# Performance work log

Hardware: AMD Instinct MI355X
Metric: run time of the kernel (lower is better)

Reference implementation:

```python
import jax, jax.numpy as jnp
import numpy as np

D_REP = 128        # node_representation_size
N_TYPES = 10000    # unique_internal_nodes (Internal_Node_Impact rows)
G = 2000           # number of external-graph nodes (internal graphs)
K = 64             # internal nodes per internal graph
DEG_IN = 8         # internal neighbour degree
DEG_EXT = 16       # external neighbour degree
B = 1024           # batch of node-id pairs


def setup_inputs() -> dict:
    key = jax.random.key(0)
    ks = jax.random.split(key, 16)
    def xavier(k, shape):
        fan_in, fan_out = shape[-1], shape[-2] if len(shape) > 1 else shape[-1]
        std = float(np.sqrt(2.0 / (fan_in + fan_out)))
        return jax.random.normal(k, shape, dtype=jnp.float32) * std
    return {
        # graph structure (integer constants)
        "batch": jax.random.randint(ks[0], (B, 2), 0, G),
        "node_type": jax.random.randint(ks[1], (G, K), 0, N_TYPES),
        "nbr_type": jax.random.randint(ks[2], (G, K, DEG_IN), 0, N_TYPES),
        "ext_nbr": jax.random.randint(ks[3], (G, DEG_EXT), 0, G),
        # InternalGraphConvolutionLayer params
        "impact": xavier(ks[4], (N_TYPES, D_REP)),   # Internal_Node_Impact
        "W": xavier(ks[5], (D_REP, D_REP)),
        "M": xavier(ks[6], (D_REP, D_REP)),
        # ExternalGraphConvolutionLayer params
        "U": xavier(ks[7], (D_REP, D_REP)),
        "V": xavier(ks[8], (D_REP, D_REP)),
        # LinkPredictionLayer params
        "W1": xavier(ks[9], (D_REP, 2 * D_REP)),
        "b1": jnp.zeros((D_REP,), dtype=jnp.float32),
        "W2": xavier(ks[10], (2, D_REP)),
        "b2": jnp.zeros((2,), dtype=jnp.float32),
    }


def reference(batch, node_type, nbr_type, ext_nbr, impact, W, M, U, V, W1, b1, W2, b2):
    # ---- InternalGraphConvolutionLayer, batched over all G graphs ----
    # per node: W @ impact[type] + sum_nbr M @ impact[nbr_type]
    self_msg = impact[node_type] @ W.T                    # [G,K,d]
    nbr_msg = impact[nbr_type].sum(axis=2) @ M.T          # gather [G,K,Din,d] -> [G,K,d]
    per_graph = jax.nn.relu(self_msg + nbr_msg).sum(axis=1)  # sum over internal nodes -> [G,d]
    E = jax.nn.softmax(per_graph, axis=-1)                # [G,d] internal embedding

    # ---- ExternalGraphConvolutionLayer, batched over all G nodes ----
    ext = E @ U.T + E[ext_nbr].sum(axis=1) @ V.T          # U@e_i + sum_j V@e_j  [G,d]
    X = jax.nn.softmax(jax.nn.relu(ext), axis=-1)         # [G,d] external embedding

    # ---- LinkPredictionLayer on each batch pair ----
    e1 = X[batch[:, 0]]                                   # [B,d]
    e2 = X[batch[:, 1]]                                   # [B,d]
    feat = jnp.concatenate([e1 * e2, e1 + e2], axis=-1)   # [B,2d]
    h = jax.nn.relu(feat @ W1.T + b1)                     # [B,d]
    return jax.nn.softmax(h @ W2.T + b2, axis=-1)         # [B,2]
```

## Files before the change

kernel.cpp:

```cpp
#include <hip/hip_runtime.h>

typedef __bf16 bf16x8 __attribute__((ext_vector_type(8)));
typedef float f32x4 __attribute__((ext_vector_type(4)));

#define G_N 2000
#define K_N 64
#define DEG_INN 8
#define DEG_EXTN 16
#define B_N 1024
#define D 128
#define NT_N 10000

__device__ __forceinline__ float bflo(unsigned int u) { return __uint_as_float(u << 16); }
__device__ __forceinline__ float bfhi(unsigned int u) { return __uint_as_float(u & 0xffff0000u); }
__device__ __forceinline__ unsigned short f2bf(float f) {
  unsigned int u = __float_as_uint(f);
  u += 0x7fffu + ((u >> 16) & 1u);
  return (unsigned short)(u >> 16);
}
__device__ __forceinline__ unsigned int pack2bf(float lo, float hi) {
  return ((unsigned int)f2bf(hi) << 16) | (unsigned int)f2bf(lo);
}

constexpr int LD1 = 136;

__global__ __launch_bounds__(256)
void k0_prep(const float* __restrict__ impact,
             const float* __restrict__ Wm, const float* __restrict__ Mm,
             const float* __restrict__ U, const float* __restrict__ V,
             const float* __restrict__ W1,
             unsigned int* __restrict__ P, unsigned int* __restrict__ Q,
             unsigned int* __restrict__ Ut, unsigned int* __restrict__ Vt,
             unsigned int* __restrict__ W1t)
{
  __shared__ __align__(16) unsigned short Bs[128 * LD1];
  __shared__ __align__(16) unsigned short As[64 * LD1];

  const int tid = threadIdx.x;

  if (blockIdx.y == 2) {
    if (blockIdx.x >= 64) return;
    const int t = blockIdx.x * 256 + tid;
    if (t < 8192) {
      int k = t >> 6, jc = t & 63;
      Ut[t] = pack2bf(U[(size_t)(2 * jc) * D + k], U[(size_t)(2 * jc + 1) * D + k]);
      Vt[t] = pack2bf(V[(size_t)(2 * jc) * D + k], V[(size_t)(2 * jc + 1) * D + k]);
    }
    {
      int k = t >> 6, jc = t & 63;
      W1t[t] = pack2bf(W1[(size_t)(2 * jc) * 256 + k], W1[(size_t)(2 * jc + 1) * 256 + k]);
    }
    return;
  }

  const int rowbase = blockIdx.x * 64;
  const float* Bsrc = blockIdx.y ? Mm : Wm;
  unsigned int* dst = blockIdx.y ? Q : P;
  const int wave = tid >> 6, lane = tid & 63;

  for (int i = tid; i < 128 * 32; i += 256) {
    int row = i >> 5, c4 = i & 31;
    float4 v = ((const float4*)Bsrc)[row * 32 + c4];
    *(unsigned int*)(Bs + row * LD1 + c4 * 4)     = pack2bf(v.x, v.y);
    *(unsigned int*)(Bs + row * LD1 + c4 * 4 + 2) = pack2bf(v.z, v.w);
  }
  for (int i = tid; i < 64 * 32; i += 256) {
    int r = i >> 5, c4 = i & 31;
    int gr = rowbase + r; if (gr > NT_N - 1) gr = NT_N - 1;
    float4 v = ((const float4*)impact)[(size_t)gr * 32 + c4];
    *(unsigned int*)(As + r * LD1 + c4 * 4)     = pack2bf(v.x, v.y);
    *(unsigned int*)(As + r * LD1 + c4 * 4 + 2) = pack2bf(v.z, v.w);
  }
  __syncthreads();

  f32x4 acc[8];
  #pragma unroll
  for (int n = 0; n < 8; ++n) acc[n] = (f32x4){0.f, 0.f, 0.f, 0.f};
  const int qk   = (lane >> 4) * 8;
  const int arow = wave * 16 + (lane & 15);
  #pragma unroll
  for (int kk = 0; kk < 4; ++kk) {
    bf16x8 af = *(const bf16x8*)(As + arow * LD1 + kk * 32 + qk);
    #pragma unroll
    for (int n = 0; n < 8; ++n) {
      bf16x8 bfr = *(const bf16x8*)(Bs + (n * 16 + (lane & 15)) * LD1 + kk * 32 + qk);
      acc[n] = __builtin_amdgcn_mfma_f32_16x16x32_bf16(af, bfr, acc[n], 0, 0, 0);
    }
  }
  __syncthreads();

  const int quad = lane >> 4, c = lane & 15;
  #pragma unroll
  for (int n = 0; n < 8; ++n)
    #pragma unroll
    for (int reg = 0; reg < 4; ++reg)
      As[(wave * 16 + quad * 4 + reg) * LD1 + n * 16 + c] = f2bf(acc[n][reg]);
  __syncthreads();

  for (int i = tid; i < 64 * 32; i += 256) {
    int r = i >> 5, cc = i & 31;
    int gr = rowbase + r;
    if (gr < NT_N) {
      dst[(size_t)gr * 64 + cc * 2]     = *(unsigned int*)(As + r * LD1 + cc * 4);
      dst[(size_t)gr * 64 + cc * 2 + 1] = *(unsigned int*)(As + r * LD1 + cc * 4 + 2);
    }
  }
}

__global__ __launch_bounds__(256)
void k1_gather(const int* __restrict__ node_type, const int* __restrict__ nbr_type,
               const uint4* __restrict__ P, const uint4* __restrict__ Q,
               float* __restrict__ E)
{
  __shared__ int nts[64];
  __shared__ int nbs[512];
  __shared__ float rg[16][132];
  __shared__ float pg[128];

  const int g    = blockIdx.x;
  const int tid  = threadIdx.x;
  const int wave = tid >> 6, lane = tid & 63;
  const int slot = lane >> 4, cl = lane & 15;

  if (tid < 64) nts[tid] = node_type[g * K_N + tid];
  nbs[tid]       = nbr_type[(size_t)g * 512 + tid];
  nbs[256 + tid] = nbr_type[(size_t)g * 512 + 256 + tid];
  __syncthreads();

  float acc[8];
  #pragma unroll
  for (int i = 0; i < 8; ++i) acc[i] = 0.f;

  for (int it = 0; it < 4; ++it) {
    const int r = wave * 16 + it * 4 + slot;
    uint4 sv = P[(size_t)nts[r] * 16 + cl];
    float rv[8];
    rv[0] = bflo(sv.x); rv[1] = bfhi(sv.x); rv[2] = bflo(sv.y); rv[3] = bfhi(sv.y);
    rv[4] = bflo(sv.z); rv[5] = bfhi(sv.z); rv[6] = bflo(sv.w); rv[7] = bfhi(sv.w);
    const int* nb = nbs + r * DEG_INN;
    #pragma unroll
    for (int d = 0; d < DEG_INN; ++d) {
      uint4 qv = Q[(size_t)nb[d] * 16 + cl];
      rv[0] += bflo(qv.x); rv[1] += bfhi(qv.x); rv[2] += bflo(qv.y); rv[3] += bfhi(qv.y);
      rv[4] += bflo(qv.z); rv[5] += bfhi(qv.z); rv[6] += bflo(qv.w); rv[7] += bfhi(qv.w);
    }
    #pragma unroll
    for (int i = 0; i < 8; ++i) acc[i] += fmaxf(rv[i], 0.f);
  }

  const int grp = wave * 4 + slot;
  #pragma unroll
  for (int i = 0; i < 8; ++i) rg[grp][cl * 8 + i] = acc[i];
  __syncthreads();

  if (tid < 128) {
    float s = 0.f;
    #pragma unroll
    for (int q = 0; q < 16; ++q) s += rg[q][tid];
    pg[tid] = s;
  }
  __syncthreads();

  if (wave == 0) {
    float v0 = pg[lane], v1 = pg[64 + lane];
    float mx = fmaxf(v0, v1);
    #pragma unroll
    for (int o = 32; o; o >>= 1) mx = fmaxf(mx, __shfl_xor(mx, o, 64));
    float e0 = __expf(v0 - mx), e1 = __expf(v1 - mx);
    float s = e0 + e1;
    #pragma unroll
    for (int o = 32; o; o >>= 1) s += __shfl_xor(s, o, 64);
    float inv = 1.f / s;
    E[(size_t)g * D + lane]      = e0 * inv;
    E[(size_t)g * D + 64 + lane] = e1 * inv;
  }
}

__global__ __launch_bounds__(256)
void k3_ext(const int* __restrict__ ext_nbr, const float* __restrict__ E,
            const unsigned int* __restrict__ Ut, const unsigned int* __restrict__ Vt,
            float* __restrict__ X)
{
  __shared__ float Ev[128], Es[128];
  __shared__ float p0[4][64], p1[4][64];
  __shared__ float scr[8];
  __shared__ int en[16];

  const int g   = blockIdx.x;
  const int tid = threadIdx.x;
  const int jc  = tid & 63, grp = tid >> 6;
  const int lane = tid & 63, wv = tid >> 6;

  if (tid < 16) en[tid] = ext_nbr[g * DEG_EXTN + tid];
  __syncthreads();

  if (tid < 128) {
    Ev[tid] = E[(size_t)g * D + tid];
  } else {
    const int j = tid - 128;
    float a = 0.f;
    #pragma unroll
    for (int d = 0; d < DEG_EXTN; ++d) a += E[(size_t)en[d] * D + j];
    Es[j] = a;
  }
  __syncthreads();

  const unsigned int* T = (grp & 2) ? Vt : Ut;
  const float* act      = (grp & 2) ? Es : Ev;
  const int k0 = (grp & 1) * 64;
  float s0 = 0.f, s1 = 0.f;
  #pragma unroll 16
  for (int k = 0; k < 64; ++k) {
    unsigned int uu = T[(k0 + k) * 64 + jc];
    float a = act[k0 + k];
    s0 += bflo(uu) * a; s1 += bfhi(uu) * a;
  }
  p0[grp][jc] = s0; p1[grp][jc] = s1;
  __syncthreads();

  float r = 0.f, e = 0.f;
  if (tid < 128) {
    const int jc2 = tid >> 1;
    float v = (tid & 1) ? (p1[0][jc2] + p1[1][jc2] + p1[2][jc2] + p1[3][jc2])
                        : (p0[0][jc2] + p0[1][jc2] + p0[2][jc2] + p0[3][jc2]);
    r = fmaxf(v, 0.f);
    float mx = r;
    #pragma unroll
    for (int o = 32; o; o >>= 1) mx = fmaxf(mx, __shfl_xor(mx, o, 64));
    if (lane == 0) scr[wv] = mx;
  }
  __syncthreads();
  if (tid < 128) {
    float mx = fmaxf(scr[0], scr[1]);
    e = __expf(r - mx);
    float sm = e;
    #pragma unroll
    for (int o = 32; o; o >>= 1) sm += __shfl_xor(sm, o, 64);
    if (lane == 0) scr[4 + wv] = sm;
  }
  __syncthreads();
  if (tid < 128) X[(size_t)g * D + tid] = e / (scr[4] + scr[5]);
}

__global__ __launch_bounds__(256)
void k4_mlp(const int* __restrict__ batch, const float* __restrict__ Xv,
            const unsigned int* __restrict__ W1t, const float* __restrict__ b1,
            const float* __restrict__ W2, const float* __restrict__ b2,
            float* __restrict__ out)
{
  __shared__ float feat[256];
  __shared__ float q0[4][64], q1[4][64];
  __shared__ float hv[128];
  __shared__ float scr[2];

  const int tid = threadIdx.x;
  const int jc = tid & 63, grp = tid >> 6;
  const int lane = tid & 63, wv = tid >> 6;

  for (int it = 0; it < 2; ++it) {
    const int b = blockIdx.x * 2 + it;
    const int i1 = batch[2 * b], i2 = batch[2 * b + 1];
    if (tid < 128) {
      float e1 = Xv[(size_t)i1 * D + tid], e2 = Xv[(size_t)i2 * D + tid];
      feat[tid]       = e1 * e2;
      feat[128 + tid] = e1 + e2;
    }
    __syncthreads();

    float s0 = 0.f, s1 = 0.f;
    #pragma unroll 16
    for (int k = 0; k < 64; ++k) {
      unsigned int uu = W1t[(grp * 64 + k) * 64 + jc];
      float a = feat[grp * 64 + k];
      s0 += bflo(uu) * a; s1 += bfhi(uu) * a;
    }
    q0[grp][jc] = s0; q1[grp][jc] = s1;
    __syncthreads();

    if (tid < 128) {
      const int jc2 = tid >> 1;
      float h = (tid & 1) ? (q1[0][jc2] + q1[1][jc2] + q1[2][jc2] + q1[3][jc2])
                          : (q0[0][jc2] + q0[1][jc2] + q0[2][jc2] + q0[3][jc2]);
      hv[tid] = fmaxf(h + b1[tid], 0.f);
    }
    __syncthreads();

    if (wv < 2) {
      float p = W2[wv * 128 + lane] * hv[lane]
              + W2[wv * 128 + 64 + lane] * hv[64 + lane];
      #pragma unroll
      for (int o = 32; o; o >>= 1) p += __shfl_xor(p, o, 64);
      if (lane == 0) scr[wv] = p + b2[wv];
    }
    __syncthreads();
    if (tid == 0) {
      float r0 = scr[0], r1 = scr[1];
      float m = fmaxf(r0, r1);
      float e0 = __expf(r0 - m), e1 = __expf(r1 - m);
      float inv = 1.f / (e0 + e1);
      out[2 * b]     = e0 * inv;
      out[2 * b + 1] = e1 * inv;
    }
    __syncthreads();
  }
}

extern "C" void kernel_launch(void* const* d_in, const int* in_sizes, int n_in,
                              void* d_out, int out_size, void* d_ws, size_t ws_size,
                              hipStream_t stream) {
  const int* batch     = (const int*)d_in[0];
  const int* node_type = (const int*)d_in[1];
  const int* nbr_type  = (const int*)d_in[2];
  const int* ext_nbr   = (const int*)d_in[3];
  const float* impact  = (const float*)d_in[4];
  const float* W       = (const float*)d_in[5];
  const float* M       = (const float*)d_in[6];
  const float* U       = (const float*)d_in[7];
  const float* V       = (const float*)d_in[8];
  const float* W1      = (const float*)d_in[9];
  const float* b1      = (const float*)d_in[10];
  const float* W2      = (const float*)d_in[11];
  const float* b2      = (const float*)d_in[12];
  float* out           = (float*)d_out;

  float* E = (float*)d_ws;
  float* X = E + (size_t)G_N * D;
  unsigned int* P   = (unsigned int*)(X + (size_t)G_N * D);
  unsigned int* Q   = P + (size_t)NT_N * 64;
  unsigned int* Ut  = Q + (size_t)NT_N * 64;
  unsigned int* Vt  = Ut + 8192;
  unsigned int* W1t = Vt + 8192;

  k0_prep<<<dim3((NT_N + 63) / 64, 3), 256, 0, stream>>>(impact, W, M, U, V, W1,
                                                         P, Q, Ut, Vt, W1t);
  k1_gather<<<G_N, 256, 0, stream>>>(node_type, nbr_type,
                                     (const uint4*)P, (const uint4*)Q, E);
  k3_ext<<<G_N, 256, 0, stream>>>(ext_nbr, E, Ut, Vt, X);
  k4_mlp<<<B_N / 2, 256, 0, stream>>>(batch, X, W1t, b1, W2, b2, out);
}
```

Before: 134.9 us.

## Fuse W/M projections per block and cache weight columns in registers

The prep kernel now loads each impact tile once and computes both the W and M projections from it, instead of launching separate blocks per matrix. The external-conv and MLP kernels keep their slice of the transposed weight matrix in 64 registers and loop over four graphs or pairs per block. The neighbour sum is also split across all 256 threads. This is meant to cut repeated global weight reads and redundant impact loads, at the cost of higher register pressure and fewer blocks in flight.

```diff
diff --git a/kernel.cpp b/kernel.cpp
--- a/kernel.cpp
+++ b/kernel.cpp
@@ -38,9 +38,8 @@
 
   const int tid = threadIdx.x;
 
-  if (blockIdx.y == 2) {
-    if (blockIdx.x >= 64) return;
-    const int t = blockIdx.x * 256 + tid;
+  if (blockIdx.x >= 157) {
+    const int t = (blockIdx.x - 157) * 256 + tid;
     if (t < 8192) {
       int k = t >> 6, jc = t & 63;
       Ut[t] = pack2bf(U[(size_t)(2 * jc) * D + k], U[(size_t)(2 * jc + 1) * D + k]);
@@ -54,16 +53,11 @@
   }
 
   const int rowbase = blockIdx.x * 64;
-  const float* Bsrc = blockIdx.y ? Mm : Wm;
-  unsigned int* dst = blockIdx.y ? Q : P;
   const int wave = tid >> 6, lane = tid & 63;
-
-  for (int i = tid; i < 128 * 32; i += 256) {
-    int row = i >> 5, c4 = i & 31;
-    float4 v = ((const float4*)Bsrc)[row * 32 + c4];
-    *(unsigned int*)(Bs + row * LD1 + c4 * 4)     = pack2bf(v.x, v.y);
-    *(unsigned int*)(Bs + row * LD1 + c4 * 4 + 2) = pack2bf(v.z, v.w);
-  }
+  const int qk   = (lane >> 4) * 8;
+  const int arow = wave * 16 + (lane & 15);
+  const int quad = lane >> 4, c = lane & 15;
+
   for (int i = tid; i < 64 * 32; i += 256) {
     int r = i >> 5, c4 = i & 31;
     int gr = rowbase + r; if (gr > NT_N - 1) gr = NT_N - 1;
@@ -71,38 +65,78 @@
     *(unsigned int*)(As + r * LD1 + c4 * 4)     = pack2bf(v.x, v.y);
     *(unsigned int*)(As + r * LD1 + c4 * 4 + 2) = pack2bf(v.z, v.w);
   }
-  __syncthreads();
-
-  f32x4 acc[8];
-  #pragma unroll
-  for (int n = 0; n < 8; ++n) acc[n] = (f32x4){0.f, 0.f, 0.f, 0.f};
-  const int qk   = (lane >> 4) * 8;
-  const int arow = wave * 16 + (lane & 15);
+  for (int i = tid; i < 128 * 32; i += 256) {
+    int row = i >> 5, c4 = i & 31;
+    float4 v = ((const float4*)Wm)[row * 32 + c4];
+    *(unsigned int*)(Bs + row * LD1 + c4 * 4)     = pack2bf(v.x, v.y);
+    *(unsigned int*)(Bs + row * LD1 + c4 * 4 + 2) = pack2bf(v.z, v.w);
+  }
+  __syncthreads();
+
+  f32x4 accW[8], accM[8];
+  #pragma unroll
+  for (int n = 0; n < 8; ++n) accW[n] = (f32x4){0.f, 0.f, 0.f, 0.f};
+  #pragma unroll
+  for (int n = 0; n < 8; ++n) accM[n] = (f32x4){0.f, 0.f, 0.f, 0.f};
+
   #pragma unroll
   for (int kk = 0; kk < 4; ++kk) {
     bf16x8 af = *(const bf16x8*)(As + arow * LD1 + kk * 32 + qk);
     #pragma unroll
     for (int n = 0; n < 8; ++n) {
       bf16x8 bfr = *(const bf16x8*)(Bs + (n * 16 + (lane & 15)) * LD1 + kk * 32 + qk);
-      acc[n] = __builtin_amdgcn_mfma_f32_16x16x32_bf16(af, bfr, acc[n], 0, 0, 0);
-    }
-  }
-  __syncthreads();
-
-  const int quad = lane >> 4, c = lane & 15;
+      accW[n] = __builtin_amdgcn_mfma_f32_16x16x32_bf16(af, bfr, accW[n], 0, 0, 0);
+    }
+  }
+  __syncthreads();
+
+  for (int i = tid; i < 128 * 32; i += 256) {
+    int row = i >> 5, c4 = i & 31;
+    float4 v = ((const float4*)Mm)[row * 32 + c4];
+    *(unsigned int*)(Bs + row * LD1 + c4 * 4)     = pack2bf(v.x, v.y);
+    *(unsigned int*)(Bs + row * LD1 + c4 * 4 + 2) = pack2bf(v.z, v.w);
+  }
+  __syncthreads();
+
+  #pragma unroll
+  for (int kk = 0; kk < 4; ++kk) {
+    bf16x8 af = *(const bf16x8*)(As + arow * LD1 + kk * 32 + qk);
+    #pragma unroll
+    for (int n = 0; n < 8; ++n) {
+      bf16x8 bfr = *(const bf16x8*)(Bs + (n * 16 + (lane & 15)) * LD1 + kk * 32 + qk);
+      accM[n] = __builtin_amdgcn_mfma_f32_16x16x32_bf16(af, bfr, accM[n], 0, 0, 0);
+    }
+  }
+  __syncthreads();
+
   #pragma unroll
   for (int n = 0; n < 8; ++n)
     #pragma unroll
     for (int reg = 0; reg < 4; ++reg)
-      As[(wave * 16 + quad * 4 + reg) * LD1 + n * 16 + c] = f2bf(acc[n][reg]);
-  __syncthreads();
-
+      As[(wave * 16 + quad * 4 + reg) * LD1 + n * 16 + c] = f2bf(accW[n][reg]);
+  __syncthreads();
   for (int i = tid; i < 64 * 32; i += 256) {
     int r = i >> 5, cc = i & 31;
     int gr = rowbase + r;
     if (gr < NT_N) {
-      dst[(size_t)gr * 64 + cc * 2]     = *(unsigned int*)(As + r * LD1 + cc * 4);
-      dst[(size_t)gr * 64 + cc * 2 + 1] = *(unsigned int*)(As + r * LD1 + cc * 4 + 2);
+      P[(size_t)gr * 64 + cc * 2]     = *(unsigned int*)(As + r * LD1 + cc * 4);
+      P[(size_t)gr * 64 + cc * 2 + 1] = *(unsigned int*)(As + r * LD1 + cc * 4 + 2);
+    }
+  }
+  __syncthreads();
+
+  #pragma unroll
+  for (int n = 0; n < 8; ++n)
+    #pragma unroll
+    for (int reg = 0; reg < 4; ++reg)
+      As[(wave * 16 + quad * 4 + reg) * LD1 + n * 16 + c] = f2bf(accM[n][reg]);
+  __syncthreads();
+  for (int i = tid; i < 64 * 32; i += 256) {
+    int r = i >> 5, cc = i & 31;
+    int gr = rowbase + r;
+    if (gr < NT_N) {
+      Q[(size_t)gr * 64 + cc * 2]     = *(unsigned int*)(As + r * LD1 + cc * 4);
+      Q[(size_t)gr * 64 + cc * 2 + 1] = *(unsigned int*)(As + r * LD1 + cc * 4 + 2);
     }
   }
 }
@@ -181,65 +215,70 @@
             const unsigned int* __restrict__ Ut, const unsigned int* __restrict__ Vt,
             float* __restrict__ X)
 {
-  __shared__ float Ev[128], Es[128];
+  __shared__ float Ev[128], EsP[2][128], Es[128];
   __shared__ float p0[4][64], p1[4][64];
   __shared__ float scr[8];
-  __shared__ int en[16];
-
-  const int g   = blockIdx.x;
+
   const int tid = threadIdx.x;
   const int jc  = tid & 63, grp = tid >> 6;
   const int lane = tid & 63, wv = tid >> 6;
 
-  if (tid < 16) en[tid] = ext_nbr[g * DEG_EXTN + tid];
-  __syncthreads();
-
-  if (tid < 128) {
-    Ev[tid] = E[(size_t)g * D + tid];
-  } else {
-    const int j = tid - 128;
-    float a = 0.f;
-    #pragma unroll
-    for (int d = 0; d < DEG_EXTN; ++d) a += E[(size_t)en[d] * D + j];
-    Es[j] = a;
-  }
-  __syncthreads();
-
   const unsigned int* T = (grp & 2) ? Vt : Ut;
-  const float* act      = (grp & 2) ? Es : Ev;
   const int k0 = (grp & 1) * 64;
-  float s0 = 0.f, s1 = 0.f;
-  #pragma unroll 16
-  for (int k = 0; k < 64; ++k) {
-    unsigned int uu = T[(k0 + k) * 64 + jc];
-    float a = act[k0 + k];
-    s0 += bflo(uu) * a; s1 += bfhi(uu) * a;
-  }
-  p0[grp][jc] = s0; p1[grp][jc] = s1;
-  __syncthreads();
-
-  float r = 0.f, e = 0.f;
-  if (tid < 128) {
-    const int jc2 = tid >> 1;
-    float v = (tid & 1) ? (p1[0][jc2] + p1[1][jc2] + p1[2][jc2] + p1[3][jc2])
-                        : (p0[0][jc2] + p0[1][jc2] + p0[2][jc2] + p0[3][jc2]);
-    r = fmaxf(v, 0.f);
-    float mx = r;
-    #pragma unroll
-    for (int o = 32; o; o >>= 1) mx = fmaxf(mx, __shfl_xor(mx, o, 64));
-    if (lane == 0) scr[wv] = mx;
-  }
-  __syncthreads();
-  if (tid < 128) {
-    float mx = fmaxf(scr[0], scr[1]);
-    e = __expf(r - mx);
-    float sm = e;
-    #pragma unroll
-    for (int o = 32; o; o >>= 1) sm += __shfl_xor(sm, o, 64);
-    if (lane == 0) scr[4 + wv] = sm;
-  }
-  __syncthreads();
-  if (tid < 128) X[(size_t)g * D + tid] = e / (scr[4] + scr[5]);
+  unsigned int Tr[64];
+  #pragma unroll
+  for (int k = 0; k < 64; ++k) Tr[k] = T[(size_t)(k0 + k) * 64 + jc];
+
+  for (int it = 0; it < 4; ++it) {
+    const int g = blockIdx.x * 4 + it;
+
+    {
+      const int j = tid & 127, h = tid >> 7;
+      float a = 0.f;
+      const int* en = ext_nbr + (size_t)g * DEG_EXTN + h * 8;
+      #pragma unroll
+      for (int d = 0; d < 8; ++d) a += E[(size_t)en[d] * D + j];
+      EsP[h][j] = a;
+      if (tid < 128) Ev[tid] = E[(size_t)g * D + tid];
+    }
+    __syncthreads();
+    if (tid < 128) Es[tid] = EsP[0][tid] + EsP[1][tid];
+    __syncthreads();
+
+    const float* act = (grp & 2) ? Es : Ev;
+    float s0 = 0.f, s1 = 0.f;
+    #pragma unroll 16
+    for (int k = 0; k < 64; ++k) {
+      float a = act[k0 + k];
+      s0 += bflo(Tr[k]) * a; s1 += bfhi(Tr[k]) * a;
+    }
+    p0[grp][jc] = s0; p1[grp][jc] = s1;
+    __syncthreads();
+
+    float r = 0.f, e = 0.f;
+    if (tid < 128) {
+      const int jc2 = tid >> 1;
+      float v = (tid & 1) ? (p1[0][jc2] + p1[1][jc2] + p1[2][jc2] + p1[3][jc2])
+                          : (p0[0][jc2] + p0[1][jc2] + p0[2][jc2] + p0[3][jc2]);
+      r = fmaxf(v, 0.f);
+      float mx = r;
+      #pragma unroll
+      for (int o = 32; o; o >>= 1) mx = fmaxf(mx, __shfl_xor(mx, o, 64));
+      if (lane == 0) scr[wv] = mx;
+    }
+    __syncthreads();
+    if (tid < 128) {
+      float mx = fmaxf(scr[0], scr[1]);
+      e = __expf(r - mx);
+      float sm = e;
+      #pragma unroll
+      for (int o = 32; o; o >>= 1) sm += __shfl_xor(sm, o, 64);
+      if (lane == 0) scr[4 + wv] = sm;
+    }
+    __syncthreads();
+    if (tid < 128) X[(size_t)g * D + tid] = e / (scr[4] + scr[5]);
+    __syncthreads();
+  }
 }
 
 __global__ __launch_bounds__(256)
@@ -257,8 +296,12 @@
   const int jc = tid & 63, grp = tid >> 6;
   const int lane = tid & 63, wv = tid >> 6;
 
-  for (int it = 0; it < 2; ++it) {
-    const int b = blockIdx.x * 2 + it;
+  unsigned int W1r[64];
+  #pragma unroll
+  for (int k = 0; k < 64; ++k) W1r[k] = W1t[(size_t)(grp * 64 + k) * 64 + jc];
+
+  for (int it = 0; it < 4; ++it) {
+    const int b = blockIdx.x * 4 + it;
     const int i1 = batch[2 * b], i2 = batch[2 * b + 1];
     if (tid < 128) {
       float e1 = Xv[(size_t)i1 * D + tid], e2 = Xv[(size_t)i2 * D + tid];
@@ -270,9 +313,8 @@
     float s0 = 0.f, s1 = 0.f;
     #pragma unroll 16
     for (int k = 0; k < 64; ++k) {
-      unsigned int uu = W1t[(grp * 64 + k) * 64 + jc];
       float a = feat[grp * 64 + k];
-      s0 += bflo(uu) * a; s1 += bfhi(uu) * a;
+      s0 += bflo(W1r[k]) * a; s1 += bfhi(W1r[k]) * a;
     }
     q0[grp][jc] = s0; q1[grp][jc] = s1;
     __syncthreads();
@@ -331,10 +373,9 @@
   unsigned int* Vt  = Ut + 8192;
   unsigned int* W1t = Vt + 8192;
 
-  k0_prep<<<dim3((NT_N + 63) / 64, 3), 256, 0, stream>>>(impact, W, M, U, V, W1,
-                                                         P, Q, Ut, Vt, W1t);
+  k0_prep<<<157 + 64, 256, 0, stream>>>(impact, W, M, U, V, W1, P, Q, Ut, Vt, W1t);
   k1_gather<<<G_N, 256, 0, stream>>>(node_type, nbr_type,
                                      (const uint4*)P, (const uint4*)Q, E);
-  k3_ext<<<G_N, 256, 0, stream>>>(ext_nbr, E, Ut, Vt, X);
-  k4_mlp<<<B_N / 2, 256, 0, stream>>>(batch, X, W1t, b1, W2, b2, out);
-}
+  k3_ext<<<G_N / 4, 256, 0, stream>>>(ext_nbr, E, Ut, Vt, X);
+  k4_mlp<<<B_N / 4, 256, 0, stream>>>(batch, X, W1t, b1, W2, b2, out);
+}
```

Result: slower. 159.1 us (+17.9%).
